# Kernel optimization log

Measured on AMD Instinct MI355X. Metric: run time of the kernel, lower is better.

The kernel has to match this reference:

```python
import jax, jax.numpy as jnp
import numpy as np

B, C, K = 1000000, 3, 64  # nodes, nb_channels (fixed=3), neighbors per node


def setup_inputs() -> dict:
    key = jax.random.key(0)
    ks = jax.random.split(key, 6)
    x = jax.random.normal(ks[0], (B, C, 1), dtype=jnp.float32)
    neighbors = jax.random.normal(ks[1], (B, C, K), dtype=jnp.float32)
    s1 = 1.0 / np.sqrt(C)        # torch Conv1d default init bound, k=1
    s2 = 1.0 / np.sqrt(C * 2)    # combine conv, kernel_size=2
    Ws = jax.random.uniform(ks[2], (C, C), jnp.float32, -s1, s1)      # self_embeding 1x1 conv weight
    bs = jax.random.uniform(ks[3], (C,), jnp.float32, -s1, s1)
    Wc = jax.random.uniform(ks[4], (C, C, 2), jnp.float32, -s2, s2)   # combine conv weight [out,in,k=2]
    bc = jax.random.uniform(ks[5], (C,), jnp.float32, -s2, s2)
    return {"x": x, "neighbors": neighbors, "Ws": Ws, "bs": bs, "Wc": Wc, "bc": bc}


def reference(x, neighbors, Ws, bs, Wc, bc):
    # self embedding: 1x1 Conv1d + Tanh on x [B, C, 1]
    h = jnp.tanh(jnp.einsum('oc,bcl->bol', Ws, x) + bs[None, :, None])  # [B, C, 1]
    # neighbor summary: avg_pool1d with kernel_size = full neighbor length.
    # NOTE: the original forward computes neighbor_embeding(neighbors) but then
    # overwrites it by pooling the RAW neighbors (and breaks after index 0), so
    # the pooled raw neighbors are what feed the combine step. Faithful to that.
    pooled = jnp.mean(neighbors, axis=2, keepdims=True)  # [B, C, 1]
    cat = jnp.concatenate([h, pooled], axis=2)  # [B, C, 2]
    # combine: Conv1d(kernel=2, stride=2) + Tanh, then final self.activation Tanh
    z = jnp.einsum('ock,bck->bo', Wc, cat) + bc[None, :]  # [B, C]
    return jnp.tanh(jnp.tanh(z))[:, :, None]  # [B, C, 1]
```

## Files before the change

### kernel.cpp

```cpp
#include <hip/hip_runtime.h>
#include <cmath>


#define THREADS 192
#define NODES_PER_BLOCK 4

__global__ __launch_bounds__(THREADS) void gnn_fused_kernel(
    const float* __restrict__ x,
    const float4* __restrict__ nbr,
    const float* __restrict__ Ws,
    const float* __restrict__ bs,
    const float* __restrict__ Wc,
    const float* __restrict__ bc,
    float* __restrict__ out,
    long long num_nodes)
{
    __shared__ float pooled[NODES_PER_BLOCK * 3];

    const int t = threadIdx.x;
    const long long gf = (long long)blockIdx.x * THREADS + t;
    const long long total_f4 = num_nodes * 48;

    float s = 0.0f;
    if (gf < total_f4) {
        float4 v = nbr[gf];
        s = (v.x + v.y) + (v.z + v.w);
    }
    s += __shfl_xor(s, 1);
    s += __shfl_xor(s, 2);
    s += __shfl_xor(s, 4);
    s += __shfl_xor(s, 8);
    if ((t & 15) == 0) pooled[t >> 4] = s * (1.0f / 64.0f);
    __syncthreads();

    if (t < NODES_PER_BLOCK * 3) {
        const int n = t / 3;
        const int o = t % 3;
        const long long node = (long long)blockIdx.x * NODES_PER_BLOCK + n;
        if (node < num_nodes) {
            const float* xp = x + node * 3;
            const float x0 = xp[0], x1 = xp[1], x2 = xp[2];
            float z = bc[o];
#pragma unroll
            for (int c = 0; c < 3; ++c) {
                float h = tanhf(Ws[c * 3 + 0] * x0 + Ws[c * 3 + 1] * x1 +
                                Ws[c * 3 + 2] * x2 + bs[c]);
                z += Wc[o * 6 + c * 2 + 0] * h +
                     Wc[o * 6 + c * 2 + 1] * pooled[n * 3 + c];
            }
            out[node * 3 + o] = tanhf(tanhf(z));
        }
    }
}

extern "C" void kernel_launch(void* const* d_in, const int* in_sizes, int n_in,
                              void* d_out, int out_size, void* d_ws, size_t ws_size,
                              hipStream_t stream) {
    const float*  x   = (const float*)d_in[0];
    const float4* nbr = (const float4*)d_in[1];
    const float*  Ws  = (const float*)d_in[2];
    const float*  bs  = (const float*)d_in[3];
    const float*  Wc  = (const float*)d_in[4];
    const float*  bc  = (const float*)d_in[5];
    float* out = (float*)d_out;

    const long long num_nodes = (long long)in_sizes[0] / 3;
    const long long blocks = (num_nodes + NODES_PER_BLOCK - 1) / NODES_PER_BLOCK;

    gnn_fused_kernel<<<(unsigned)blocks, THREADS, 0, stream>>>(
        x, nbr, Ws, bs, Wc, bc, out, num_nodes);
}
```

Measured before the change: 993.7 us.

## Process 128 nodes per block with looped loads and cooperative epilogue

Each block now handles 32 iterations of 4 nodes, looping over float4 neighbor loads with shuffle reductions into a larger shared pooled buffer. x values are staged into shared memory with coalesced loads, and all threads share the epilogue instead of only 12. This cuts the block count and the share of idle threads in the tanh tail. The cost is fewer blocks in flight and serial loads per thread, which could reduce memory-level parallelism.

```diff
diff --git a/kernel.cpp b/kernel.cpp
--- a/kernel.cpp
+++ b/kernel.cpp
@@ -3,7 +3,8 @@
 
 
 #define THREADS 192
-#define NODES_PER_BLOCK 4
+#define NITER   32
+#define NPB     (4 * NITER)
 
 __global__ __launch_bounds__(THREADS) void gnn_fused_kernel(
     const float* __restrict__ x,
@@ -15,36 +16,51 @@
     float* __restrict__ out,
     long long num_nodes)
 {
-    __shared__ float pooled[NODES_PER_BLOCK * 3];
+    __shared__ float pooled[NPB * 3];
+    __shared__ float xs[NPB * 3];
 
     const int t = threadIdx.x;
-    const long long gf = (long long)blockIdx.x * THREADS + t;
-    const long long total_f4 = num_nodes * 48;
+    const long long node_base = (long long)blockIdx.x * NPB;
+    const long long f4_base   = node_base * 48;
+    const long long total_f4  = num_nodes * 48;
+    const long long total_xf  = num_nodes * 3;
 
-    float s = 0.0f;
-    if (gf < total_f4) {
-        float4 v = nbr[gf];
-        s = (v.x + v.y) + (v.z + v.w);
+#pragma unroll
+    for (int j = t; j < NPB * 3; j += THREADS) {
+        const long long gx = node_base * 3 + j;
+        xs[j] = (gx < total_xf) ? x[gx] : 0.0f;
     }
-    s += __shfl_xor(s, 1);
-    s += __shfl_xor(s, 2);
-    s += __shfl_xor(s, 4);
-    s += __shfl_xor(s, 8);
-    if ((t & 15) == 0) pooled[t >> 4] = s * (1.0f / 64.0f);
+
+#pragma unroll 4
+    for (int it = 0; it < NITER; ++it) {
+        const long long gf = f4_base + (long long)(it * THREADS + t);
+        float s = 0.0f;
+        if (gf < total_f4) {
+            const float4 v = nbr[gf];
+            s = (v.x + v.y) + (v.z + v.w);
+        }
+        s += __shfl_xor(s, 1);
+        s += __shfl_xor(s, 2);
+        s += __shfl_xor(s, 4);
+        s += __shfl_xor(s, 8);
+        if ((t & 15) == 0) pooled[it * 12 + (t >> 4)] = s * (1.0f / 64.0f);
+    }
     __syncthreads();
 
-    if (t < NODES_PER_BLOCK * 3) {
-        const int n = t / 3;
-        const int o = t % 3;
-        const long long node = (long long)blockIdx.x * NODES_PER_BLOCK + n;
+#pragma unroll
+    for (int j = t; j < NPB * 3; j += THREADS) {
+        const int n = j / 3;
+        const int o = j - n * 3;
+        const long long node = node_base + n;
         if (node < num_nodes) {
-            const float* xp = x + node * 3;
-            const float x0 = xp[0], x1 = xp[1], x2 = xp[2];
+            const float x0 = xs[n * 3 + 0];
+            const float x1 = xs[n * 3 + 1];
+            const float x2 = xs[n * 3 + 2];
             float z = bc[o];
 #pragma unroll
             for (int c = 0; c < 3; ++c) {
-                float h = tanhf(Ws[c * 3 + 0] * x0 + Ws[c * 3 + 1] * x1 +
-                                Ws[c * 3 + 2] * x2 + bs[c]);
+                const float h = tanhf(Ws[c * 3 + 0] * x0 + Ws[c * 3 + 1] * x1 +
+                                      Ws[c * 3 + 2] * x2 + bs[c]);
                 z += Wc[o * 6 + c * 2 + 0] * h +
                      Wc[o * 6 + c * 2 + 1] * pooled[n * 3 + c];
             }
@@ -65,7 +81,7 @@
     float* out = (float*)d_out;
 
     const long long num_nodes = (long long)in_sizes[0] / 3;
-    const long long blocks = (num_nodes + NODES_PER_BLOCK - 1) / NODES_PER_BLOCK;
+    const long long blocks = (num_nodes + NPB - 1) / NPB;
 
     gnn_fused_kernel<<<(unsigned)blocks, THREADS, 0, stream>>>(
         x, nbr, Ws, bs, Wc, bc, out, num_nodes);
```

New measurement: 983.3 us. Within noise of the previous version (-1.1%).
